# Kernel tuning notes

Measured on AMD Instinct MI355X. Metric: run time of the kernel, lower is better.

## Reference

```python
import jax, jax.numpy as jnp
import numpy as np

L, B, FC, SC = 256, 32, 64, 64
SIGMA = 2.0
W_T, W_S = 0.5, 0.5  # w_temporal, w_spatial


def _decays(seq_len, sigma):
    # K[s, i] = exp(-(s-i)^2 / (2 sigma^2))
    t = jnp.arange(seq_len, dtype=jnp.float32)
    K = jnp.exp(-(t[:, None] - t[None, :]) ** 2 / (2.0 * sigma * sigma))
    # past: average over i < s (divide by s); row s=0 is all zeros
    past = jnp.tril(K, -1) / jnp.maximum(t, 1.0)[:, None]
    # future: average over i > s (divide by L-1-s); row s=L-1 is all zeros
    fut = jnp.triu(K, 1) / jnp.maximum(seq_len - 1.0 - t, 1.0)[:, None]
    return past, fut


def _ce(logits, labels):
    # mean cross entropy over rows, labels: int (N,)
    lg = jax.nn.log_softmax(logits, axis=-1)
    return -jnp.mean(jnp.take_along_axis(lg, labels[:, None], axis=-1))


def setup_inputs() -> dict:
    key = jax.random.key(0)
    ks = jax.random.split(key, 9)
    return {
        "f": jax.random.normal(ks[0], (L, B, FC), jnp.float32),
        "s": jax.random.normal(ks[1], (L, B, SC), jnp.float32),
        "fs": jax.random.normal(ks[2], (L, B, FC, SC), jnp.float32),
        "ff": jax.random.normal(ks[3], (L, B, FC, FC), jnp.float32),
        "ss": jax.random.normal(ks[4], (L, B, SC, SC), jnp.float32),
        "fs_t": jax.random.normal(ks[5], (L, B, FC, SC), jnp.float32),
        "sf_t": jax.random.normal(ks[6], (L, B, SC, FC), jnp.float32),
        "f_labels": jax.random.randint(ks[7], (L * B,), 0, FC),
        "s_labels": jax.random.randint(ks[8], (L * B,), 0, SC),
    }


def reference(f, s, fs, ff, ss, fs_t, sf_t, f_labels, s_labels):
    past, fut = _decays(L, SIGMA)
    loss = _ce(f.reshape(-1, FC), f_labels) + _ce(s.reshape(-1, SC), s_labels)
    prev_f, prev_s = f, s
    # --- one mean-field message passing iteration (training mode) ---
    # gaussian-weighted averaged past/future messages: (L,L) @ (L,B,C)
    f_mp = jnp.einsum('si,ibc->sbc', past, prev_f)
    f_mf = jnp.einsum('si,ibc->sbc', fut, prev_f)
    s_mp = jnp.einsum('si,ibc->sbc', past, prev_s)
    s_mf = jnp.einsum('si,ibc->sbc', fut, prev_s)
    next_f = (f
              + W_T * (jnp.einsum('lbf,lbfg->lbg', f_mp, ff)
                       + jnp.einsum('lbfg,lbg->lbf', ff, f_mf)
                       + jnp.einsum('lbs,lbsf->lbf', s_mp, sf_t)
                       + jnp.einsum('lbfs,lbs->lbf', fs_t, s_mf))
              + W_S * jnp.einsum('lbfs,lbs->lbf', fs, prev_s))
    next_s = (s
              + W_T * (jnp.einsum('lbs,lbst->lbt', s_mp, ss)
                       + jnp.einsum('lbst,lbt->lbs', ss, s_mf)
                       + jnp.einsum('lbf,lbfs->lbs', f_mp, fs_t)
                       + jnp.einsum('lbsf,lbf->lbs', sf_t, f_mf))
              + W_S * jnp.einsum('lbf,lbfs->lbs', prev_f, fs))
    loss = loss + _ce(next_f.reshape(-1, FC), f_labels) + _ce(next_s.reshape(-1, SC), s_labels)
    f_out = jax.nn.softmax(next_f, axis=-1)
    s_out = jax.nn.softmax(next_s, axis=-1)
    return f_out, s_out, loss
```

## Files before the change

kernel.cpp:

```cpp
#include <hip/hip_runtime.h>
#include <math.h>

#define Lseq 256
#define Bn   32
#define Cn   64
#define WIN  22

__global__ void zero_loss_kernel(float* p) { *p = 0.0f; }

__device__ __forceinline__ void mat_pass(
    const float4* __restrict__ M4,
    const float* __restrict__ vrow, const float* __restrict__ vcol,
    float* outA, float* outB, float wA, float wB,
    float* stage , int tid)
{
  const int cb = tid & 15;
  const int m  = tid >> 4;
  const float vc0 = vcol[4*cb+0], vc1 = vcol[4*cb+1];
  const float vc2 = vcol[4*cb+2], vc3 = vcol[4*cb+3];
  float pA0 = 0.f, pA1 = 0.f, pA2 = 0.f, pA3 = 0.f;
  float pB[4];
#pragma unroll
  for (int k = 0; k < 4; ++k) {
    float4 v = M4[tid + 256*k];
    float vr = vrow[m + 16*k];
    pA0 += vr * v.x; pA1 += vr * v.y; pA2 += vr * v.z; pA3 += vr * v.w;
    pB[k] = v.x*vc0 + v.y*vc1 + v.z*vc2 + v.w*vc3;
  }
  reinterpret_cast<float4*>(stage)[m*16 + cb] = make_float4(pA0, pA1, pA2, pA3);
#pragma unroll
  for (int k = 0; k < 4; ++k) {
#pragma unroll
    for (int off = 8; off >= 1; off >>= 1)
      pB[k] += __shfl_xor(pB[k], off, 64);
  }
  if (cb == 0) {
#pragma unroll
    for (int k = 0; k < 4; ++k)
      outB[m + 16*k] += wB * pB[k];
  }
  __syncthreads();
  if (tid < 64) {
    float acc = 0.f;
#pragma unroll
    for (int mm = 0; mm < 16; ++mm) acc += stage[mm*64 + tid];
    outA[tid] += wA * acc;
  }
  __syncthreads();
}

__global__ __launch_bounds__(256) void tf_criterion_kernel(
    const float* __restrict__ f,   const float* __restrict__ s,
    const float* __restrict__ fs,  const float* __restrict__ ff,
    const float* __restrict__ ss,  const float* __restrict__ fs_t,
    const float* __restrict__ sf_t,
    const int* __restrict__ f_labels, const int* __restrict__ s_labels,
    float* __restrict__ out)
{
  __shared__ float4 stage4[256];
  __shared__ float f_mp[64], f_mf[64], s_mp[64], s_mf[64];
  __shared__ float prev_f[64], prev_s[64];
  __shared__ float nf[64], ns[64];
  __shared__ float lp[4];

  const int tid = threadIdx.x;
  const int lb  = blockIdx.x;
  const int l   = lb >> 5;
  const int b   = lb & 31;

  if (tid < 128) {
    const int which = tid >> 6;
    const int c     = tid & 63;
    const float* src = which ? s : f;
    float mp = 0.f, mf = 0.f, pv = 0.f;
    int i0 = l - WIN; if (i0 < 0) i0 = 0;
    int i1 = l + WIN; if (i1 > Lseq - 1) i1 = Lseq - 1;
    for (int i = i0; i <= i1; ++i) {
      float x = src[((size_t)i * Bn + b) * Cn + c];
      int d = l - i;
      if (d == 0) { pv = x; continue; }
      float w = expf(-0.125f * (float)(d * d));
      if (d > 0) mp += w * x; else mf += w * x;
    }
    mp *= 1.0f / (float)((l > 1) ? l : 1);
    mf *= 1.0f / (float)((Lseq - 1 - l > 1) ? (Lseq - 1 - l) : 1);
    if (which == 0) { f_mp[c] = mp; f_mf[c] = mf; prev_f[c] = pv; }
    else            { s_mp[c] = mp; s_mf[c] = mf; prev_s[c] = pv; }
  } else if (tid < 192) {
    nf[tid - 128] = 0.f;
  } else {
    ns[tid - 192] = 0.f;
  }
  __syncthreads();

  float* stage = reinterpret_cast<float*>(stage4);
  const size_t mo = (size_t)lb * 4096;
  mat_pass((const float4*)(ff   + mo), f_mp,   f_mf,   nf, nf, 0.5f, 0.5f, stage, tid);
  mat_pass((const float4*)(ss   + mo), s_mp,   s_mf,   ns, ns, 0.5f, 0.5f, stage, tid);
  mat_pass((const float4*)(sf_t + mo), s_mp,   f_mf,   nf, ns, 0.5f, 0.5f, stage, tid);
  mat_pass((const float4*)(fs_t + mo), f_mp,   s_mf,   ns, nf, 0.5f, 0.5f, stage, tid);
  mat_pass((const float4*)(fs   + mo), prev_f, prev_s, ns, nf, 0.5f, 0.5f, stage, tid);

  const int w = tid >> 6;
  const int c = tid & 63;
  float x;
  if      (w == 0) x = prev_f[c];
  else if (w == 1) x = prev_s[c];
  else if (w == 2) x = prev_f[c] + nf[c];
  else             x = prev_s[c] + ns[c];

  float mx = x;
#pragma unroll
  for (int off = 32; off >= 1; off >>= 1)
    mx = fmaxf(mx, __shfl_xor(mx, off, 64));
  float e  = expf(x - mx);
  float sm = e;
#pragma unroll
  for (int off = 32; off >= 1; off >>= 1)
    sm += __shfl_xor(sm, off, 64);

  if      (w == 2) out[(size_t)lb * 64 + c]          = e / sm;
  else if (w == 3) out[524288 + (size_t)lb * 64 + c] = e / sm;

  float lse = logf(sm) + mx;
  int lab = (w & 1) ? s_labels[lb] : f_labels[lb];
  if (c == lab) lp[w] = lse - x;
  __syncthreads();
  if (tid == 0)
    atomicAdd(out + 1048576, (lp[0] + lp[1] + lp[2] + lp[3]) * (1.0f / 8192.0f));
}

extern "C" void kernel_launch(void* const* d_in, const int* in_sizes, int n_in,
                              void* d_out, int out_size, void* d_ws, size_t ws_size,
                              hipStream_t stream) {
  const float* f     = (const float*)d_in[0];
  const float* s     = (const float*)d_in[1];
  const float* fs    = (const float*)d_in[2];
  const float* ff    = (const float*)d_in[3];
  const float* ss    = (const float*)d_in[4];
  const float* fs_t  = (const float*)d_in[5];
  const float* sf_t  = (const float*)d_in[6];
  const int*   f_lab = (const int*)d_in[7];
  const int*   s_lab = (const int*)d_in[8];
  float* out = (float*)d_out;

  zero_loss_kernel<<<1, 1, 0, stream>>>(out + 1048576);
  tf_criterion_kernel<<<Lseq * Bn, 256, 0, stream>>>(
      f, s, fs, ff, ss, fs_t, sf_t, f_lab, s_lab, out);
}
```

Measured before the change: 548.8 us.

## Prefetch all five matrices up front and fuse matvec passes into one reduction

The five per-(l,b) 64x64 matrices are now loaded into registers at kernel start, before the Gaussian window reduction, so global loads overlap with the message computation. The five separate matvec passes, each ending in two barriers, are merged into a single pass that accumulates the nf and ns contributions together, with one shared-memory reduction per output. The window loop is split across all 256 threads (past and future handled by separate groups) and fully unrolled with branch-free bounds handling. This costs about 80 extra registers per thread, with launch bounds set to 4 blocks per SM, which risks spilling.

```diff
diff --git a/kernel.cpp b/kernel.cpp
--- a/kernel.cpp
+++ b/kernel.cpp
@@ -8,48 +8,7 @@
 
 __global__ void zero_loss_kernel(float* p) { *p = 0.0f; }
 
-__device__ __forceinline__ void mat_pass(
-    const float4* __restrict__ M4,
-    const float* __restrict__ vrow, const float* __restrict__ vcol,
-    float* outA, float* outB, float wA, float wB,
-    float* stage , int tid)
-{
-  const int cb = tid & 15;
-  const int m  = tid >> 4;
-  const float vc0 = vcol[4*cb+0], vc1 = vcol[4*cb+1];
-  const float vc2 = vcol[4*cb+2], vc3 = vcol[4*cb+3];
-  float pA0 = 0.f, pA1 = 0.f, pA2 = 0.f, pA3 = 0.f;
-  float pB[4];
-#pragma unroll
-  for (int k = 0; k < 4; ++k) {
-    float4 v = M4[tid + 256*k];
-    float vr = vrow[m + 16*k];
-    pA0 += vr * v.x; pA1 += vr * v.y; pA2 += vr * v.z; pA3 += vr * v.w;
-    pB[k] = v.x*vc0 + v.y*vc1 + v.z*vc2 + v.w*vc3;
-  }
-  reinterpret_cast<float4*>(stage)[m*16 + cb] = make_float4(pA0, pA1, pA2, pA3);
-#pragma unroll
-  for (int k = 0; k < 4; ++k) {
-#pragma unroll
-    for (int off = 8; off >= 1; off >>= 1)
-      pB[k] += __shfl_xor(pB[k], off, 64);
-  }
-  if (cb == 0) {
-#pragma unroll
-    for (int k = 0; k < 4; ++k)
-      outB[m + 16*k] += wB * pB[k];
-  }
-  __syncthreads();
-  if (tid < 64) {
-    float acc = 0.f;
-#pragma unroll
-    for (int mm = 0; mm < 16; ++mm) acc += stage[mm*64 + tid];
-    outA[tid] += wA * acc;
-  }
-  __syncthreads();
-}
-
-__global__ __launch_bounds__(256) void tf_criterion_kernel(
+__global__ __launch_bounds__(256, 4) void tf_criterion_kernel(
     const float* __restrict__ f,   const float* __restrict__ s,
     const float* __restrict__ fs,  const float* __restrict__ ff,
     const float* __restrict__ ss,  const float* __restrict__ fs_t,
@@ -57,57 +16,135 @@
     const int* __restrict__ f_labels, const int* __restrict__ s_labels,
     float* __restrict__ out)
 {
-  __shared__ float4 stage4[256];
-  __shared__ float f_mp[64], f_mf[64], s_mp[64], s_mf[64];
-  __shared__ float prev_f[64], prev_s[64];
-  __shared__ float nf[64], ns[64];
+  __shared__ __align__(16) float stageNF[1024];
+  __shared__ __align__(16) float stageNS[1024];
+  __shared__ __align__(16) float f_mp[64], f_mf[64], s_mp[64], s_mf[64];
+  __shared__ __align__(16) float prev_f[64], prev_s[64];
+  __shared__ float nfR[64], nsR[64];
+  __shared__ float nfv[64], nsv[64];
   __shared__ float lp[4];
 
   const int tid = threadIdx.x;
   const int lb  = blockIdx.x;
   const int l   = lb >> 5;
   const int b   = lb & 31;
+  const int cb  = tid & 15;
+  const int m   = tid >> 4;
 
-  if (tid < 128) {
-    const int which = tid >> 6;
-    const int c     = tid & 63;
-    const float* src = which ? s : f;
-    float mp = 0.f, mf = 0.f, pv = 0.f;
-    int i0 = l - WIN; if (i0 < 0) i0 = 0;
-    int i1 = l + WIN; if (i1 > Lseq - 1) i1 = Lseq - 1;
-    for (int i = i0; i <= i1; ++i) {
-      float x = src[((size_t)i * Bn + b) * Cn + c];
-      int d = l - i;
-      if (d == 0) { pv = x; continue; }
-      float w = expf(-0.125f * (float)(d * d));
-      if (d > 0) mp += w * x; else mf += w * x;
+  const size_t mo = (size_t)lb * 4096;
+  const float4* M_ff = (const float4*)(ff   + mo);
+  const float4* M_ss = (const float4*)(ss   + mo);
+  const float4* M_sf = (const float4*)(sf_t + mo);
+  const float4* M_ft = (const float4*)(fs_t + mo);
+  const float4* M_fs = (const float4*)(fs   + mo);
+  float4 v_ff[4], v_ss[4], v_sf[4], v_ft[4], v_fs[4];
+#pragma unroll
+  for (int k = 0; k < 4; ++k) v_ff[k] = M_ff[tid + 256*k];
+#pragma unroll
+  for (int k = 0; k < 4; ++k) v_ss[k] = M_ss[tid + 256*k];
+#pragma unroll
+  for (int k = 0; k < 4; ++k) v_sf[k] = M_sf[tid + 256*k];
+#pragma unroll
+  for (int k = 0; k < 4; ++k) v_ft[k] = M_ft[tid + 256*k];
+#pragma unroll
+  for (int k = 0; k < 4; ++k) v_fs[k] = M_fs[tid + 256*k];
+
+  {
+    const int grp = tid >> 6;
+    const int c   = tid & 63;
+    const float* src = (grp & 2) ? s : f;
+    float acc = 0.f;
+    if ((grp & 1) == 0) {
+#pragma unroll
+      for (int j = 1; j <= WIN; ++j) {
+        int i = l - j;
+        bool valid = (i >= 0);
+        float w = valid ? expf(-0.125f * (float)(j * j)) : 0.f;
+        int idx = valid ? i : 0;
+        acc += w * src[((size_t)idx * Bn + b) * Cn + c];
+      }
+      acc *= 1.0f / (float)((l > 1) ? l : 1);
+      float pv = src[((size_t)l * Bn + b) * Cn + c];
+      if (grp == 0) { f_mp[c] = acc; prev_f[c] = pv; }
+      else          { s_mp[c] = acc; prev_s[c] = pv; }
+    } else {
+#pragma unroll
+      for (int j = 1; j <= WIN; ++j) {
+        int i = l + j;
+        bool valid = (i <= Lseq - 1);
+        float w = valid ? expf(-0.125f * (float)(j * j)) : 0.f;
+        int idx = valid ? i : 0;
+        acc += w * src[((size_t)idx * Bn + b) * Cn + c];
+      }
+      acc *= 1.0f / (float)((Lseq - 1 - l > 1) ? (Lseq - 1 - l) : 1);
+      if (grp == 1) f_mf[c] = acc; else s_mf[c] = acc;
     }
-    mp *= 1.0f / (float)((l > 1) ? l : 1);
-    mf *= 1.0f / (float)((Lseq - 1 - l > 1) ? (Lseq - 1 - l) : 1);
-    if (which == 0) { f_mp[c] = mp; f_mf[c] = mf; prev_f[c] = pv; }
-    else            { s_mp[c] = mp; s_mf[c] = mf; prev_s[c] = pv; }
-  } else if (tid < 192) {
-    nf[tid - 128] = 0.f;
-  } else {
-    ns[tid - 192] = 0.f;
   }
   __syncthreads();
 
-  float* stage = reinterpret_cast<float*>(stage4);
-  const size_t mo = (size_t)lb * 4096;
-  mat_pass((const float4*)(ff   + mo), f_mp,   f_mf,   nf, nf, 0.5f, 0.5f, stage, tid);
-  mat_pass((const float4*)(ss   + mo), s_mp,   s_mf,   ns, ns, 0.5f, 0.5f, stage, tid);
-  mat_pass((const float4*)(sf_t + mo), s_mp,   f_mf,   nf, ns, 0.5f, 0.5f, stage, tid);
-  mat_pass((const float4*)(fs_t + mo), f_mp,   s_mf,   ns, nf, 0.5f, 0.5f, stage, tid);
-  mat_pass((const float4*)(fs   + mo), prev_f, prev_s, ns, nf, 0.5f, 0.5f, stage, tid);
+  float accNF[4] = {0,0,0,0}, accNS[4] = {0,0,0,0};
+  float rowNF[4] = {0,0,0,0}, rowNS[4] = {0,0,0,0};
+  const float4 c_fmf = ((const float4*)f_mf)[cb];
+  const float4 c_smf = ((const float4*)s_mf)[cb];
+  const float4 c_ps  = ((const float4*)prev_s)[cb];
+
+#pragma unroll
+  for (int k = 0; k < 4; ++k) {
+    const int r = m + 16*k;
+    const float vfp = f_mp[r], vsp = s_mp[r], vpf = prev_f[r];
+    { float4 v = v_ff[k];
+      accNF[0]+=vfp*v.x; accNF[1]+=vfp*v.y; accNF[2]+=vfp*v.z; accNF[3]+=vfp*v.w;
+      rowNF[k]+= v.x*c_fmf.x + v.y*c_fmf.y + v.z*c_fmf.z + v.w*c_fmf.w; }
+    { float4 v = v_ss[k];
+      accNS[0]+=vsp*v.x; accNS[1]+=vsp*v.y; accNS[2]+=vsp*v.z; accNS[3]+=vsp*v.w;
+      rowNS[k]+= v.x*c_smf.x + v.y*c_smf.y + v.z*c_smf.z + v.w*c_smf.w; }
+    { float4 v = v_sf[k];
+      accNF[0]+=vsp*v.x; accNF[1]+=vsp*v.y; accNF[2]+=vsp*v.z; accNF[3]+=vsp*v.w;
+      rowNS[k]+= v.x*c_fmf.x + v.y*c_fmf.y + v.z*c_fmf.z + v.w*c_fmf.w; }
+    { float4 v = v_ft[k];
+      accNS[0]+=vfp*v.x; accNS[1]+=vfp*v.y; accNS[2]+=vfp*v.z; accNS[3]+=vfp*v.w;
+      rowNF[k]+= v.x*c_smf.x + v.y*c_smf.y + v.z*c_smf.z + v.w*c_smf.w; }
+    { float4 v = v_fs[k];
+      accNS[0]+=vpf*v.x; accNS[1]+=vpf*v.y; accNS[2]+=vpf*v.z; accNS[3]+=vpf*v.w;
+      rowNF[k]+= v.x*c_ps.x + v.y*c_ps.y + v.z*c_ps.z + v.w*c_ps.w; }
+  }
+
+#pragma unroll
+  for (int k = 0; k < 4; ++k) {
+#pragma unroll
+    for (int off = 8; off >= 1; off >>= 1) {
+      rowNF[k] += __shfl_xor(rowNF[k], off, 64);
+      rowNS[k] += __shfl_xor(rowNS[k], off, 64);
+    }
+  }
+  if (cb == 0) {
+#pragma unroll
+    for (int k = 0; k < 4; ++k) { nfR[m+16*k] = rowNF[k]; nsR[m+16*k] = rowNS[k]; }
+  }
+  reinterpret_cast<float4*>(stageNF)[m*16 + cb] =
+      make_float4(accNF[0], accNF[1], accNF[2], accNF[3]);
+  reinterpret_cast<float4*>(stageNS)[m*16 + cb] =
+      make_float4(accNS[0], accNS[1], accNS[2], accNS[3]);
+  __syncthreads();
+
+  if (tid < 128) {
+    const int c = tid & 63;
+    const float* stg = (tid < 64) ? stageNF : stageNS;
+    float acc = 0.f;
+#pragma unroll
+    for (int mm = 0; mm < 16; ++mm) acc += stg[mm*64 + c];
+    if (tid < 64) nfv[c] = prev_f[c] + 0.5f * (acc + nfR[c]);
+    else          nsv[c] = prev_s[c] + 0.5f * (acc + nsR[c]);
+  }
+  __syncthreads();
 
   const int w = tid >> 6;
   const int c = tid & 63;
   float x;
   if      (w == 0) x = prev_f[c];
   else if (w == 1) x = prev_s[c];
-  else if (w == 2) x = prev_f[c] + nf[c];
-  else             x = prev_s[c] + ns[c];
+  else if (w == 2) x = nfv[c];
+  else             x = nsv[c];
 
   float mx = x;
 #pragma unroll
```

After: 561.6 us. +2.3%, slower.

## Precompute Gaussian past/future messages in a separate coalesced kernel

Applied to the files above, without the earlier changes.

Adds a pre-pass kernel that computes the windowed Gaussian past and future averages for f and s across all positions with fully parallel, coalesced loads, and writes them to workspace. The main kernel then loads these precomputed messages instead of having 128 threads each walk a 45-step serial loop before the matrix passes. The aim is to shorten the latency-bound prologue of every block. The cost is an extra launch and roughly 8 MB of workspace writes and reads. The old path stays as a fallback when the workspace is too small.

```diff
diff --git a/kernel.cpp b/kernel.cpp
--- a/kernel.cpp
+++ b/kernel.cpp
@@ -7,6 +7,39 @@
 #define WIN  22
 
 __global__ void zero_loss_kernel(float* p) { *p = 0.0f; }
+
+__global__ __launch_bounds__(256) void msg_kernel(
+    const float* __restrict__ f, const float* __restrict__ s,
+    float* __restrict__ fmp, float* __restrict__ fmf,
+    float* __restrict__ smp, float* __restrict__ smf)
+{
+  const int bid = blockIdx.x;
+  const int l   = bid >> 3;
+  const int p   = ((bid & 7) << 8) + threadIdx.x;
+  const size_t base = (size_t)l * 2048 + p;
+
+  float fp = 0.f, fu = 0.f, sp = 0.f, su = 0.f;
+#pragma unroll
+  for (int j = 1; j <= WIN; ++j) {
+    const float w = expf(-0.125f * (float)(j * j));
+    const int ip = l - j;
+    if (ip >= 0) {
+      fp += w * f[(size_t)ip * 2048 + p];
+      sp += w * s[(size_t)ip * 2048 + p];
+    }
+    const int iq = l + j;
+    if (iq < Lseq) {
+      fu += w * f[(size_t)iq * 2048 + p];
+      su += w * s[(size_t)iq * 2048 + p];
+    }
+  }
+  const float rp = 1.0f / (float)((l > 1) ? l : 1);
+  const float rf = 1.0f / (float)((Lseq - 1 - l > 1) ? (Lseq - 1 - l) : 1);
+  fmp[base] = fp * rp;
+  fmf[base] = fu * rf;
+  smp[base] = sp * rp;
+  smf[base] = su * rf;
+}
 
 __device__ __forceinline__ void mat_pass(
     const float4* __restrict__ M4,
@@ -54,8 +87,10 @@
     const float* __restrict__ fs,  const float* __restrict__ ff,
     const float* __restrict__ ss,  const float* __restrict__ fs_t,
     const float* __restrict__ sf_t,
+    const float* __restrict__ fmp_g, const float* __restrict__ fmf_g,
+    const float* __restrict__ smp_g, const float* __restrict__ smf_g,
     const int* __restrict__ f_labels, const int* __restrict__ s_labels,
-    float* __restrict__ out)
+    float* __restrict__ out, int use_msgs)
 {
   __shared__ float4 stage4[256];
   __shared__ float f_mp[64], f_mf[64], s_mp[64], s_mf[64];
@@ -68,28 +103,45 @@
   const int l   = lb >> 5;
   const int b   = lb & 31;
 
-  if (tid < 128) {
-    const int which = tid >> 6;
-    const int c     = tid & 63;
-    const float* src = which ? s : f;
-    float mp = 0.f, mf = 0.f, pv = 0.f;
-    int i0 = l - WIN; if (i0 < 0) i0 = 0;
-    int i1 = l + WIN; if (i1 > Lseq - 1) i1 = Lseq - 1;
-    for (int i = i0; i <= i1; ++i) {
-      float x = src[((size_t)i * Bn + b) * Cn + c];
-      int d = l - i;
-      if (d == 0) { pv = x; continue; }
-      float w = expf(-0.125f * (float)(d * d));
-      if (d > 0) mp += w * x; else mf += w * x;
-    }
-    mp *= 1.0f / (float)((l > 1) ? l : 1);
-    mf *= 1.0f / (float)((Lseq - 1 - l > 1) ? (Lseq - 1 - l) : 1);
-    if (which == 0) { f_mp[c] = mp; f_mf[c] = mf; prev_f[c] = pv; }
-    else            { s_mp[c] = mp; s_mf[c] = mf; prev_s[c] = pv; }
-  } else if (tid < 192) {
-    nf[tid - 128] = 0.f;
+  if (use_msgs) {
+    if (tid < 128) {
+      const int which = tid >> 6;
+      const int c     = tid & 63;
+      const size_t base = (size_t)lb * 64 + c;
+      if (which == 0) {
+        f_mp[c] = fmp_g[base]; f_mf[c] = fmf_g[base]; prev_f[c] = f[base];
+      } else {
+        s_mp[c] = smp_g[base]; s_mf[c] = smf_g[base]; prev_s[c] = s[base];
+      }
+    } else if (tid < 192) {
+      nf[tid - 128] = 0.f;
+    } else {
+      ns[tid - 192] = 0.f;
+    }
   } else {
-    ns[tid - 192] = 0.f;
+    if (tid < 128) {
+      const int which = tid >> 6;
+      const int c     = tid & 63;
+      const float* src = which ? s : f;
+      float mp = 0.f, mf = 0.f, pv = 0.f;
+      int i0 = l - WIN; if (i0 < 0) i0 = 0;
+      int i1 = l + WIN; if (i1 > Lseq - 1) i1 = Lseq - 1;
+      for (int i = i0; i <= i1; ++i) {
+        float x = src[((size_t)i * Bn + b) * Cn + c];
+        int d = l - i;
+        if (d == 0) { pv = x; continue; }
+        float w = expf(-0.125f * (float)(d * d));
+        if (d > 0) mp += w * x; else mf += w * x;
+      }
+      mp *= 1.0f / (float)((l > 1) ? l : 1);
+      mf *= 1.0f / (float)((Lseq - 1 - l > 1) ? (Lseq - 1 - l) : 1);
+      if (which == 0) { f_mp[c] = mp; f_mf[c] = mf; prev_f[c] = pv; }
+      else            { s_mp[c] = mp; s_mf[c] = mf; prev_s[c] = pv; }
+    } else if (tid < 192) {
+      nf[tid - 128] = 0.f;
+    } else {
+      ns[tid - 192] = 0.f;
+    }
   }
   __syncthreads();
 
@@ -144,7 +196,19 @@
   const int*   s_lab = (const int*)d_in[8];
   float* out = (float*)d_out;
 
+  const size_t msg_elems = (size_t)Lseq * Bn * Cn;
+  const size_t ws_needed = 4 * msg_elems * sizeof(float);
+  const int use_msgs = (d_ws != nullptr && ws_size >= ws_needed) ? 1 : 0;
+
+  float* fmp = (float*)d_ws;
+  float* fmf = fmp + msg_elems;
+  float* smp = fmf + msg_elems;
+  float* smf = smp + msg_elems;
+
   zero_loss_kernel<<<1, 1, 0, stream>>>(out + 1048576);
+  if (use_msgs)
+    msg_kernel<<<Lseq * 8, 256, 0, stream>>>(f, s, fmp, fmf, smp, smf);
   tf_criterion_kernel<<<Lseq * Bn, 256, 0, stream>>>(
-      f, s, fs, ff, ss, fs_t, sf_t, f_lab, s_lab, out);
-}
+      f, s, fs, ff, ss, fs_t, sf_t, fmp, fmf, smp, smf, f_lab, s_lab, out,
+      use_msgs);
+}
```

After: 560.8 us. 2.2% more time.
